# Kernel tuning notes

Measured on AMD Instinct MI355X. Metric: run time of the kernel, lower is better.

The kernel has to match this reference:

```python
import jax, jax.numpy as jnp
import numpy as np

# Module config (init_kwargs)
OUT_H, OUT_W = 7, 7
SPATIAL_SCALE = 0.25
SAMPLE_NUM = 2          # fixed sampling grid (sample_num > 0 branch of mmcv kernel)
ALIGNED = True
CLOCKWISE = False

B, C, H, W = 2, 256, 200, 200
R = 1000


def setup_inputs() -> dict:
    key = jax.random.key(0)
    k1, k2, k3, k4, k5, k6 = jax.random.split(key, 6)
    features = jax.random.normal(k1, (B, C, H, W), dtype=jnp.float32)
    # rois: (batch_index, cx, cy, w, h, angle) in input-image coordinates
    bidx = jax.random.randint(k2, (R,), 0, B).astype(jnp.float32)
    cx = jax.random.uniform(k3, (R,), minval=100.0, maxval=700.0)
    cy = jax.random.uniform(k4, (R,), minval=100.0, maxval=700.0)
    wh = jax.random.uniform(k5, (R, 2), minval=20.0, maxval=200.0)
    ang = jax.random.uniform(k6, (R,), minval=-np.pi, maxval=np.pi)
    rois = jnp.concatenate(
        [bidx[:, None], cx[:, None], cy[:, None], wh, ang[:, None]], axis=1
    ).astype(jnp.float32)
    return {"features": features, "rois": rois}


def _bilinear_gather(features, bidx, y, x):
    """features: [B,C,H,W]; bidx: [R] int; y,x: [R,P] float. Returns [R,P,C]."""
    Hf, Wf = features.shape[2], features.shape[3]
    valid = (y > -1.0) & (y < Hf) & (x > -1.0) & (x < Wf)
    y = jnp.maximum(y, 0.0)
    x = jnp.maximum(x, 0.0)
    yl = jnp.floor(y).astype(jnp.int32)
    xl = jnp.floor(x).astype(jnp.int32)
    ych = yl >= Hf - 1
    xch = xl >= Wf - 1
    yl = jnp.where(ych, Hf - 1, yl)
    yh = jnp.where(ych, Hf - 1, yl + 1)
    xl = jnp.where(xch, Wf - 1, xl)
    xh = jnp.where(xch, Wf - 1, xl + 1)
    ly = jnp.where(ych, 0.0, y - yl.astype(y.dtype))
    lx = jnp.where(xch, 0.0, x - xl.astype(x.dtype))
    hy, hx = 1.0 - ly, 1.0 - lx
    b = bidx[:, None]  # [R,1] broadcast against [R,P]
    v1 = features[b, :, yl, xl]  # [R,P,C]
    v2 = features[b, :, yl, xh]
    v3 = features[b, :, yh, xl]
    v4 = features[b, :, yh, xh]
    val = (hy * hx)[..., None] * v1 + (hy * lx)[..., None] * v2 \
        + (ly * hx)[..., None] * v3 + (ly * lx)[..., None] * v4
    return jnp.where(valid[..., None], val, 0.0)


def _roi_align_rotated(features, rois):
    g = SAMPLE_NUM
    offset = 0.5 if ALIGNED else 0.0
    bidx = rois[:, 0].astype(jnp.int32)
    cx = rois[:, 1] * SPATIAL_SCALE - offset
    cy = rois[:, 2] * SPATIAL_SCALE - offset
    rw = rois[:, 3] * SPATIAL_SCALE
    rh = rois[:, 4] * SPATIAL_SCALE
    theta = -rois[:, 5] if CLOCKWISE else rois[:, 5]
    if not ALIGNED:
        rw = jnp.maximum(rw, 1.0)
        rh = jnp.maximum(rh, 1.0)
    bin_h = rh / OUT_H
    bin_w = rw / OUT_W
    # sample offsets within roi frame, origin at roi center
    ph = jnp.arange(OUT_H, dtype=jnp.float32)
    pw = jnp.arange(OUT_W, dtype=jnp.float32)
    ig = (jnp.arange(g, dtype=jnp.float32) + 0.5) / g
    # yy: [R, OUT_H, g]; xx: [R, OUT_W, g]
    yy = -rh[:, None, None] / 2.0 + (ph[None, :, None] + ig[None, None, :]) * bin_h[:, None, None]
    xx = -rw[:, None, None] / 2.0 + (pw[None, :, None] + ig[None, None, :]) * bin_w[:, None, None]
    # broadcast to [R, OUT_H, OUT_W, g, g]
    yy5 = yy[:, :, None, :, None]
    xx5 = xx[:, None, :, None, :]
    sin_t = jnp.sin(theta)[:, None, None, None, None]
    cos_t = jnp.cos(theta)[:, None, None, None, None]
    x = yy5 * sin_t + xx5 * cos_t + cx[:, None, None, None, None]
    y = yy5 * cos_t - xx5 * sin_t + cy[:, None, None, None, None]
    P = OUT_H * OUT_W * g * g
    vals = _bilinear_gather(features, bidx, y.reshape(R, P), x.reshape(R, P))  # [R,P,C]
    vals = vals.reshape(R, OUT_H, OUT_W, g * g, C).mean(axis=3)  # [R,OUT_H,OUT_W,C]
    return jnp.transpose(vals, (0, 3, 1, 2))  # [R,C,OUT_H,OUT_W]


def reference(features, rois):
    return _roi_align_rotated(features, rois)
```

## Files before the change

### kernel.cpp

```cpp
#include <hip/hip_runtime.h>
#include <math.h>

#define OUT_H 7
#define OUT_W 7
#define GS 2
#define NBINS (OUT_H * OUT_W)
#define NSAMP (GS * GS)
#define NMETA (NBINS * NSAMP)
#define SPATIAL_SCALE 0.25f
#define B_ 2
#define C_ 256
#define H_ 200
#define W_ 200
#define R_ 1000
#define HW_ (H_ * W_)

typedef _Float16 half_t;
typedef __attribute__((ext_vector_type(8))) _Float16 half8;
typedef __attribute__((ext_vector_type(2))) _Float16 half2_t;
typedef __attribute__((ext_vector_type(4))) float f32x4;


__global__ __launch_bounds__(256)
void nchw_to_nhwc_h(const float* __restrict__ in, half_t* __restrict__ out,
                    const float* __restrict__ rois, int* __restrict__ perm) {
    __shared__ float tile[64][64];

    __shared__ int bpos[8][64];
    __shared__ int novf, take;
    __shared__ unsigned char claimed[R_];
    __shared__ short ovf[R_];
    if (blockIdx.x == 0 && blockIdx.y == 0 && blockIdx.z == 0) {
        const int t0 = threadIdx.x;
        for (int i = t0; i < 8 * 64; i += 256) ((int*)bpos)[i] = 0;
        if (t0 == 0) { novf = 0; take = 0; }
        for (int t = t0; t < R_; t += 256) claimed[t] = 0;
        __syncthreads();
        for (int t = t0; t < R_; t += 256) {
            const float* roi = rois + t * 6;
            int   b   = (int)roi[0];
            float cyf = roi[2] * SPATIAL_SCALE;
            float cxf = roi[1] * SPATIAL_SCALE;
            int q = (int)((cyf - 25.0f) * (4.0f / 150.0f));
            q = q < 0 ? 0 : (q > 3 ? 3 : q);
            int band = b * 4 + q;
            band = band < 0 ? 0 : (band > 7 ? 7 : band);
            int bk = (int)((cxf - 25.0f) * (64.0f / 150.0f));
            bk = bk < 0 ? 0 : (bk > 63 ? 63 : bk);
            atomicAdd(&bpos[band][bk], 1);
        }
        __syncthreads();
        if (t0 < 8) {
            int s = 0;
            for (int k = 0; k < 64; ++k) {
                int c = bpos[t0][k];
                bpos[t0][k] = s;
                s += c;
            }
        }
        __syncthreads();
        for (int t = t0; t < R_; t += 256) {
            const float* roi = rois + t * 6;
            int   b   = (int)roi[0];
            float cyf = roi[2] * SPATIAL_SCALE;
            float cxf = roi[1] * SPATIAL_SCALE;
            int q = (int)((cyf - 25.0f) * (4.0f / 150.0f));
            q = q < 0 ? 0 : (q > 3 ? 3 : q);
            int band = b * 4 + q;
            band = band < 0 ? 0 : (band > 7 ? 7 : band);
            int bk = (int)((cxf - 25.0f) * (64.0f / 150.0f));
            bk = bk < 0 ? 0 : (bk > 63 ? 63 : bk);
            int pos = atomicAdd(&bpos[band][bk], 1);
            if (pos < R_ / 8) {
                int id = band + 8 * pos;
                perm[id] = t;
                claimed[id] = 1;
            } else {
                ovf[atomicAdd(&novf, 1)] = (short)t;
            }
        }
        __syncthreads();
        for (int t = t0; t < R_; t += 256) {
            if (!claimed[t]) perm[t] = (int)ovf[atomicAdd(&take, 1)];
        }
    }

    const int hw0 = blockIdx.x * 64;
    const int c0  = blockIdx.y * 64;
    const int b   = blockIdx.z;
    const int t   = threadIdx.x;

    {
        const f32x4* ip4 = (const f32x4*)(in + ((size_t)b * C_ + c0) * HW_ + hw0);
        const int r = t >> 4;
        const int q = t & 15;
#pragma unroll
        for (int k = 0; k < 4; ++k) {
            const int c = r + 16 * k;
            f32x4 v = __builtin_nontemporal_load(&ip4[(size_t)c * (HW_ / 4) + q]);
            const int g = q ^ ((c ^ (c >> 3)) & 7);
            ((f32x4*)tile)[c * 16 + g] = v;
        }
    }
    __syncthreads();
    {
        const int cg = t & 7;
        const int hb = t >> 3;
        half_t* op = out + ((size_t)b * HW_ + hw0) * C_ + c0 + 8 * cg;
#pragma unroll
        for (int i = 0; i < 2; ++i) {
            const int hw = hb + 32 * i;
            const int gh = hw >> 2, oh = hw & 3;
            half8 h;
#pragma unroll
            for (int dc = 0; dc < 8; ++dc) {
                const int c = 8 * cg + dc;
                const float f = tile[c][4 * (gh ^ ((c ^ (c >> 3)) & 7)) + oh];
                h[dc] = (half_t)f;
            }
            *(half8*)(op + (size_t)hw * C_) = h;
        }
    }
}

__device__ __forceinline__ void mix2(float& a0, float& a1,
                                     unsigned int pair, float w) {
    asm("v_fma_mix_f32 %0, %1, %2, %0 op_sel:[0,0,0] op_sel_hi:[1,0,0]"
        : "+v"(a0) : "v"(pair), "v"(w));
    asm("v_fma_mix_f32 %0, %1, %2, %0 op_sel:[1,0,0] op_sel_hi:[1,0,0]"
        : "+v"(a1) : "v"(pair), "v"(w));
}

__device__ __forceinline__ void mix8(float (&a)[8], const uint4& t, float w) {
    mix2(a[0], a[1], t.x, w); mix2(a[2], a[3], t.y, w);
    mix2(a[4], a[5], t.z, w); mix2(a[6], a[7], t.w, w);
}

struct TapsP { uint4 t[8]; };

__device__ __forceinline__ void load_pairs(TapsP& T, const uint4* __restrict__ fp4,
                                           const int2* __restrict__ s_o,
                                           int m, int lane) {
#pragma unroll
    for (int s = 0; s < 4; ++s) {
        const int2 o = s_o[m + s];
        T.t[2 * s + 0] = fp4[o.x + lane];
        T.t[2 * s + 1] = fp4[o.y + lane];
    }
}

__device__ __forceinline__ void fma_store(const TapsP& T,
                                          const float4* __restrict__ s_w,
                                          int m, int j, int lane,
                                          float (&obuf)[8][32][NBINS]) {
    float a[8] = {0.f, 0.f, 0.f, 0.f, 0.f, 0.f, 0.f, 0.f};
    const float2* w2 = ((const float2*)s_w) + (lane >> 5);
#pragma unroll
    for (int s = 0; s < 4; ++s) {
        const float2 ws = w2[2 * (m + s)];
        mix8(a, T.t[2 * s + 0], ws.x);
        mix8(a, T.t[2 * s + 1], ws.y);
    }
#pragma unroll
    for (int k = 0; k < 8; ++k) a[k] += __shfl_xor(a[k], 32, 64);
    if (lane < 32) {
#pragma unroll
        for (int k = 0; k < 8; ++k) obuf[k][lane][j] = a[k];
    }
}

__global__ __launch_bounds__(512, 4)
void gather_nhwc(const half_t* __restrict__ nhwc,
                 const float* __restrict__ rois,
                 const int* __restrict__ perm,
                 float* __restrict__ out) {
    __shared__ float  obuf[8][32][NBINS];
    __shared__ int2   s_o[NMETA];
    __shared__ float4 s_w[NMETA];

    const int r    = perm[blockIdx.x];
    const int tid  = threadIdx.x;
    const int wave = tid >> 6;
    const int lane = tid & 63;

    if (tid < NMETA) {
        const float* roi = rois + r * 6;
        const int   b     = (int)roi[0];
        const float cx    = roi[1] * SPATIAL_SCALE - 0.5f;
        const float cy    = roi[2] * SPATIAL_SCALE - 0.5f;
        const float rw    = roi[3] * SPATIAL_SCALE;
        const float rh    = roi[4] * SPATIAL_SCALE;
        const float theta = roi[5];
        const float bin_h = rh * (1.0f / OUT_H);
        const float bin_w = rw * (1.0f / OUT_W);
        float st, ct;
        __sincosf(theta, &st, &ct);

        const int bin = tid >> 2;
        const int s   = tid & 3;
        const int ph  = bin / OUT_W, pw = bin % OUT_W;
        const int iy  = s >> 1,      ix = s & 1;

        const float yy = -rh * 0.5f + ((float)ph + ((float)iy + 0.5f) * 0.5f) * bin_h;
        const float xx = -rw * 0.5f + ((float)pw + ((float)ix + 0.5f) * 0.5f) * bin_w;
        float x = yy * st + xx * ct + cx;
        float y = yy * ct - xx * st + cy;

        const bool valid = (y > -1.0f) && (y < (float)H_) &&
                           (x > -1.0f) && (x < (float)W_);
        y = fmaxf(y, 0.0f);
        x = fmaxf(x, 0.0f);
        int yl = (int)y, xl = (int)x;
        int yh; float ly;
        if (yl >= H_ - 1) { yl = H_ - 1; yh = H_ - 1; ly = 0.0f; }
        else              { yh = yl + 1; ly = y - (float)yl; }
        int xp; float e0, e1;
        if (xl >= W_ - 1) { xp = W_ - 2; e0 = 0.0f; e1 = 1.0f; }
        else              { xp = xl; const float lx = x - (float)xl;
                            e0 = 1.0f - lx; e1 = lx; }
        const float hy = 1.0f - ly;
        const float scale = valid ? (1.0f / NSAMP) : 0.0f;

        const int bplane = b * HW_;
        s_o[tid] = make_int2((bplane + yl * W_ + xp) * 32,
                             (bplane + yh * W_ + xp) * 32);
        s_w[tid] = make_float4(hy * e0 * scale, ly * e0 * scale,
                               hy * e1 * scale, ly * e1 * scale);
    }
    __syncthreads();

    const uint4* __restrict__ fp4 = (const uint4*)nhwc;

    {
        TapsP A, B;
        int jA = wave;
        int jB = wave + 8;
        load_pairs(A, fp4, s_o, 4 * jA, lane);
        if (jB < NBINS) load_pairs(B, fp4, s_o, 4 * jB, lane);
        __builtin_amdgcn_sched_barrier(0);

        fma_store(A, s_w, 4 * jA, jA, lane, obuf);
        jA += 16;
        if (jA < NBINS) load_pairs(A, fp4, s_o, 4 * jA, lane);
        __builtin_amdgcn_sched_barrier(0);
        if (jB < NBINS) {
            fma_store(B, s_w, 4 * jB, jB, lane, obuf);
            jB += 16;
            if (jB < NBINS) load_pairs(B, fp4, s_o, 4 * jB, lane);
            __builtin_amdgcn_sched_barrier(0);
        }
        if (jA < NBINS) {
            fma_store(A, s_w, 4 * jA, jA, lane, obuf);
            jA += 16;
            if (jA < NBINS) load_pairs(A, fp4, s_o, 4 * jA, lane);
            __builtin_amdgcn_sched_barrier(0);
        }
        if (jB < NBINS) {
            fma_store(B, s_w, 4 * jB, jB, lane, obuf);
            jB += 16;
            if (jB < NBINS) load_pairs(B, fp4, s_o, 4 * jB, lane);
            __builtin_amdgcn_sched_barrier(0);
        }
        if (jA < NBINS) {
            fma_store(A, s_w, 4 * jA, jA, lane, obuf);
            jA += 16;
            if (jA < NBINS) load_pairs(A, fp4, s_o, 4 * jA, lane);
            __builtin_amdgcn_sched_barrier(0);
        }
        if (jB < NBINS) {
            fma_store(B, s_w, 4 * jB, jB, lane, obuf);
            jB += 16;
        }
        if (jA < NBINS) {
            fma_store(A, s_w, 4 * jA, jA, lane, obuf);
        }
    }
    __syncthreads();

    float* out_r = out + (size_t)r * (C_ * NBINS);
    const int E = C_ * NBINS;
#pragma unroll
    for (int i = 0; i < (E + 511) / 512; ++i) {
        const int f = tid + 512 * i;
        if (f < E) {
            const int c = f / NBINS;
            const int j = f - c * NBINS;
            __builtin_nontemporal_store(obuf[c & 7][c >> 3][j], &out_r[f]);
        }
    }
}


struct alignas(16) Samp {
    int o0, o1, o2, o3;
    float w0, w1, w2, w3;
};

__device__ __forceinline__ Samp compute_samp(const float* __restrict__ rois,
                                             int r, int ph, int pw, int s) {
    const float* roi = rois + r * 6;
    int   b     = (int)roi[0];
    float cx    = roi[1] * SPATIAL_SCALE - 0.5f;
    float cy    = roi[2] * SPATIAL_SCALE - 0.5f;
    float rw    = roi[3] * SPATIAL_SCALE;
    float rh    = roi[4] * SPATIAL_SCALE;
    float theta = roi[5];
    float bin_h = rh * (1.0f / OUT_H);
    float bin_w = rw * (1.0f / OUT_W);
    int iy = s / GS, ix = s % GS;
    float yy = -rh * 0.5f + ((float)ph + ((float)iy + 0.5f) * (1.0f / GS)) * bin_h;
    float xx = -rw * 0.5f + ((float)pw + ((float)ix + 0.5f) * (1.0f / GS)) * bin_w;
    float st = sinf(theta), ct = cosf(theta);
    float x = yy * st + xx * ct + cx;
    float y = yy * ct - xx * st + cy;
    bool valid = (y > -1.0f) && (y < (float)H_) && (x > -1.0f) && (x < (float)W_);
    y = fmaxf(y, 0.0f);
    x = fmaxf(x, 0.0f);
    int yl = (int)y;
    int xl = (int)x;
    int yh; float ly;
    if (yl >= H_ - 1) { yl = H_ - 1; yh = H_ - 1; ly = 0.0f; }
    else              { yh = yl + 1; ly = y - (float)yl; }
    int xh; float lx;
    if (xl >= W_ - 1) { xl = W_ - 1; xh = W_ - 1; lx = 0.0f; }
    else              { xh = xl + 1; lx = x - (float)xl; }
    float hy = 1.0f - ly, hx = 1.0f - lx;
    float scale = valid ? (1.0f / NSAMP) : 0.0f;
    Samp sp;
    int base = b * (C_ * H_ * W_);
    sp.o0 = base + yl * W_ + xl;
    sp.o1 = base + yl * W_ + xh;
    sp.o2 = base + yh * W_ + xl;
    sp.o3 = base + yh * W_ + xh;
    sp.w0 = hy * hx * scale;
    sp.w1 = hy * lx * scale;
    sp.w2 = ly * hx * scale;
    sp.w3 = ly * lx * scale;
    return sp;
}

__global__ __launch_bounds__(256)
void mono_kernel(const float* __restrict__ feat,
                 const float* __restrict__ rois,
                 float* __restrict__ out) {
    int tid = blockIdx.x * blockDim.x + threadIdx.x;
    if (tid >= R_ * C_ * NBINS) return;
    int bin = tid % NBINS;
    int rc  = tid / NBINS;
    int c   = rc % C_;
    int r   = rc / C_;
    int coff = c * (H_ * W_);
    float acc = 0.0f;
#pragma unroll
    for (int s = 0; s < NSAMP; ++s) {
        Samp t = compute_samp(rois, r, bin / OUT_W, bin % OUT_W, s);
        acc += t.w0 * feat[coff + t.o0];
        acc += t.w1 * feat[coff + t.o1];
        acc += t.w2 * feat[coff + t.o2];
        acc += t.w3 * feat[coff + t.o3];
    }
    out[tid] = acc;
}


extern "C" void kernel_launch(void* const* d_in, const int* in_sizes, int n_in,
                              void* d_out, int out_size, void* d_ws, size_t ws_size,
                              hipStream_t stream) {
    const float* feat = (const float*)d_in[0];
    const float* rois = (const float*)d_in[1];
    float* out = (float*)d_out;

    const size_t nhwc_bytes = (size_t)B_ * C_ * HW_ * sizeof(half_t);
    const size_t perm_bytes = (size_t)R_ * sizeof(int);

    if (ws_size >= nhwc_bytes + perm_bytes) {
        half_t* nhwc = (half_t*)d_ws;
        int*    perm = (int*)((char*)d_ws + nhwc_bytes);
        dim3 tgrid(HW_ / 64, C_ / 64, B_);
        nchw_to_nhwc_h<<<tgrid, 256, 0, stream>>>(feat, nhwc, rois, perm);
        gather_nhwc<<<R_, 512, 0, stream>>>(nhwc, rois, perm, out);
    } else {
        const int n_out = R_ * C_ * NBINS;
        mono_kernel<<<(n_out + 255) / 256, 256, 0, stream>>>(feat, rois, out);
    }
}
```

Measured before the change: 151.6 us.

## Deduplicate and skip zero-weight bilinear row taps per bin

Per-sample metadata is replaced by per-bin metadata: one thread per output bin computes its four sample points, merges taps that share a row-pair address, and drops taps whose weights are both zero. Only the unique non-zero taps are fetched and accumulated. The goal is fewer global gathers for out-of-bounds or overlapping samples in small ROIs. The cost is a serial dedup loop in 49 threads, variable-length loops with data-dependent branches, and the loss of the explicit software-pipelined double buffering across bins.

```diff
diff --git a/kernel.cpp b/kernel.cpp
--- a/kernel.cpp
+++ b/kernel.cpp
@@ -6,7 +6,6 @@
 #define GS 2
 #define NBINS (OUT_H * OUT_W)
 #define NSAMP (GS * GS)
-#define NMETA (NBINS * NSAMP)
 #define SPATIAL_SCALE 0.25f
 #define B_ 2
 #define C_ 256
@@ -136,54 +135,22 @@
     mix2(a[4], a[5], t.z, w); mix2(a[6], a[7], t.w, w);
 }
 
-struct TapsP { uint4 t[8]; };
-
-__device__ __forceinline__ void load_pairs(TapsP& T, const uint4* __restrict__ fp4,
-                                           const int2* __restrict__ s_o,
-                                           int m, int lane) {
-#pragma unroll
-    for (int s = 0; s < 4; ++s) {
-        const int2 o = s_o[m + s];
-        T.t[2 * s + 0] = fp4[o.x + lane];
-        T.t[2 * s + 1] = fp4[o.y + lane];
-    }
-}
-
-__device__ __forceinline__ void fma_store(const TapsP& T,
-                                          const float4* __restrict__ s_w,
-                                          int m, int j, int lane,
-                                          float (&obuf)[8][32][NBINS]) {
-    float a[8] = {0.f, 0.f, 0.f, 0.f, 0.f, 0.f, 0.f, 0.f};
-    const float2* w2 = ((const float2*)s_w) + (lane >> 5);
-#pragma unroll
-    for (int s = 0; s < 4; ++s) {
-        const float2 ws = w2[2 * (m + s)];
-        mix8(a, T.t[2 * s + 0], ws.x);
-        mix8(a, T.t[2 * s + 1], ws.y);
-    }
-#pragma unroll
-    for (int k = 0; k < 8; ++k) a[k] += __shfl_xor(a[k], 32, 64);
-    if (lane < 32) {
-#pragma unroll
-        for (int k = 0; k < 8; ++k) obuf[k][lane][j] = a[k];
-    }
-}
-
 __global__ __launch_bounds__(512, 4)
 void gather_nhwc(const half_t* __restrict__ nhwc,
                  const float* __restrict__ rois,
                  const int* __restrict__ perm,
                  float* __restrict__ out) {
     __shared__ float  obuf[8][32][NBINS];
-    __shared__ int2   s_o[NMETA];
-    __shared__ float4 s_w[NMETA];
+    __shared__ int    s_cnt[NBINS];
+    __shared__ int    s_off[NBINS][8];
+    __shared__ float2 s_w[NBINS][8];
 
     const int r    = perm[blockIdx.x];
     const int tid  = threadIdx.x;
     const int wave = tid >> 6;
     const int lane = tid & 63;
 
-    if (tid < NMETA) {
+    if (tid < NBINS) {
         const float* roi = rois + r * 6;
         const int   b     = (int)roi[0];
         const float cx    = roi[1] * SPATIAL_SCALE - 0.5f;
@@ -196,83 +163,101 @@
         float st, ct;
         __sincosf(theta, &st, &ct);
 
-        const int bin = tid >> 2;
-        const int s   = tid & 3;
-        const int ph  = bin / OUT_W, pw = bin % OUT_W;
-        const int iy  = s >> 1,      ix = s & 1;
-
-        const float yy = -rh * 0.5f + ((float)ph + ((float)iy + 0.5f) * 0.5f) * bin_h;
-        const float xx = -rw * 0.5f + ((float)pw + ((float)ix + 0.5f) * 0.5f) * bin_w;
-        float x = yy * st + xx * ct + cx;
-        float y = yy * ct - xx * st + cy;
-
-        const bool valid = (y > -1.0f) && (y < (float)H_) &&
-                           (x > -1.0f) && (x < (float)W_);
-        y = fmaxf(y, 0.0f);
-        x = fmaxf(x, 0.0f);
-        int yl = (int)y, xl = (int)x;
-        int yh; float ly;
-        if (yl >= H_ - 1) { yl = H_ - 1; yh = H_ - 1; ly = 0.0f; }
-        else              { yh = yl + 1; ly = y - (float)yl; }
-        int xp; float e0, e1;
-        if (xl >= W_ - 1) { xp = W_ - 2; e0 = 0.0f; e1 = 1.0f; }
-        else              { xp = xl; const float lx = x - (float)xl;
-                            e0 = 1.0f - lx; e1 = lx; }
-        const float hy = 1.0f - ly;
-        const float scale = valid ? (1.0f / NSAMP) : 0.0f;
-
+        const int ph = tid / OUT_W, pw = tid % OUT_W;
         const int bplane = b * HW_;
-        s_o[tid] = make_int2((bplane + yl * W_ + xp) * 32,
-                             (bplane + yh * W_ + xp) * 32);
-        s_w[tid] = make_float4(hy * e0 * scale, ly * e0 * scale,
-                               hy * e1 * scale, ly * e1 * scale);
+
+        int   offs[8];
+        float w0a[8], w1a[8];
+        int n = 0;
+#pragma unroll
+        for (int s = 0; s < NSAMP; ++s) {
+            const int iy = s >> 1, ix = s & 1;
+            const float yy = -rh * 0.5f + ((float)ph + ((float)iy + 0.5f) * 0.5f) * bin_h;
+            const float xx = -rw * 0.5f + ((float)pw + ((float)ix + 0.5f) * 0.5f) * bin_w;
+            float x = yy * st + xx * ct + cx;
+            float y = yy * ct - xx * st + cy;
+
+            const bool valid = (y > -1.0f) && (y < (float)H_) &&
+                               (x > -1.0f) && (x < (float)W_);
+            y = fmaxf(y, 0.0f);
+            x = fmaxf(x, 0.0f);
+            int yl = (int)y, xl = (int)x;
+            int yh; float ly;
+            if (yl >= H_ - 1) { yl = H_ - 1; yh = H_ - 1; ly = 0.0f; }
+            else              { yh = yl + 1; ly = y - (float)yl; }
+            int xp; float e0, e1;
+            if (xl >= W_ - 1) { xp = W_ - 2; e0 = 0.0f; e1 = 1.0f; }
+            else              { xp = xl; const float lx = x - (float)xl;
+                                e0 = 1.0f - lx; e1 = lx; }
+            const float hy = 1.0f - ly;
+            const float scale = valid ? (1.0f / NSAMP) : 0.0f;
+
+            const int   ro[2] = { (bplane + yl * W_ + xp) * 32,
+                                  (bplane + yh * W_ + xp) * 32 };
+            const float wy[2] = { hy, ly };
+            for (int h = 0; h < 2; ++h) {
+                const float w0 = wy[h] * e0 * scale;
+                const float w1 = wy[h] * e1 * scale;
+                if (w0 == 0.0f && w1 == 0.0f) continue;
+                int f = -1;
+                for (int k = 0; k < n; ++k)
+                    if (offs[k] == ro[h]) { f = k; break; }
+                if (f >= 0) { w0a[f] += w0; w1a[f] += w1; }
+                else        { offs[n] = ro[h]; w0a[n] = w0; w1a[n] = w1; ++n; }
+            }
+        }
+        s_cnt[tid] = n;
+        for (int k = 0; k < n; ++k) {
+            s_off[tid][k] = offs[k];
+            s_w[tid][k]   = make_float2(w0a[k], w1a[k]);
+        }
     }
     __syncthreads();
 
     const uint4* __restrict__ fp4 = (const uint4*)nhwc;
 
-    {
-        TapsP A, B;
-        int jA = wave;
-        int jB = wave + 8;
-        load_pairs(A, fp4, s_o, 4 * jA, lane);
-        if (jB < NBINS) load_pairs(B, fp4, s_o, 4 * jB, lane);
+    for (int j = wave; j < NBINS; j += 16) {
+        const int j2 = j + 8;
+        const int nA = s_cnt[j];
+        const int nB = (j2 < NBINS) ? s_cnt[j2] : 0;
+        uint4 tA[8], tB[8];
+#pragma unroll
+        for (int k = 0; k < 8; ++k)
+            if (k < nA) tA[k] = fp4[s_off[j][k] + lane];
+#pragma unroll
+        for (int k = 0; k < 8; ++k)
+            if (k < nB) tB[k] = fp4[s_off[j2][k] + lane];
         __builtin_amdgcn_sched_barrier(0);
 
-        fma_store(A, s_w, 4 * jA, jA, lane, obuf);
-        jA += 16;
-        if (jA < NBINS) load_pairs(A, fp4, s_o, 4 * jA, lane);
-        __builtin_amdgcn_sched_barrier(0);
-        if (jB < NBINS) {
-            fma_store(B, s_w, 4 * jB, jB, lane, obuf);
-            jB += 16;
-            if (jB < NBINS) load_pairs(B, fp4, s_o, 4 * jB, lane);
-            __builtin_amdgcn_sched_barrier(0);
-        }
-        if (jA < NBINS) {
-            fma_store(A, s_w, 4 * jA, jA, lane, obuf);
-            jA += 16;
-            if (jA < NBINS) load_pairs(A, fp4, s_o, 4 * jA, lane);
-            __builtin_amdgcn_sched_barrier(0);
-        }
-        if (jB < NBINS) {
-            fma_store(B, s_w, 4 * jB, jB, lane, obuf);
-            jB += 16;
-            if (jB < NBINS) load_pairs(B, fp4, s_o, 4 * jB, lane);
-            __builtin_amdgcn_sched_barrier(0);
-        }
-        if (jA < NBINS) {
-            fma_store(A, s_w, 4 * jA, jA, lane, obuf);
-            jA += 16;
-            if (jA < NBINS) load_pairs(A, fp4, s_o, 4 * jA, lane);
-            __builtin_amdgcn_sched_barrier(0);
-        }
-        if (jB < NBINS) {
-            fma_store(B, s_w, 4 * jB, jB, lane, obuf);
-            jB += 16;
-        }
-        if (jA < NBINS) {
-            fma_store(A, s_w, 4 * jA, jA, lane, obuf);
+        {
+            float a[8] = {0.f, 0.f, 0.f, 0.f, 0.f, 0.f, 0.f, 0.f};
+#pragma unroll
+            for (int k = 0; k < 8; ++k)
+                if (k < nA) {
+                    const float2 w = s_w[j][k];
+                    mix8(a, tA[k], (lane & 32) ? w.y : w.x);
+                }
+#pragma unroll
+            for (int k = 0; k < 8; ++k) a[k] += __shfl_xor(a[k], 32, 64);
+            if (lane < 32) {
+#pragma unroll
+                for (int k = 0; k < 8; ++k) obuf[k][lane][j] = a[k];
+            }
+        }
+        if (j2 < NBINS) {
+            float a[8] = {0.f, 0.f, 0.f, 0.f, 0.f, 0.f, 0.f, 0.f};
+#pragma unroll
+            for (int k = 0; k < 8; ++k)
+                if (k < nB) {
+                    const float2 w = s_w[j2][k];
+                    mix8(a, tB[k], (lane & 32) ? w.y : w.x);
+                }
+#pragma unroll
+            for (int k = 0; k < 8; ++k) a[k] += __shfl_xor(a[k], 32, 64);
+            if (lane < 32) {
+#pragma unroll
+                for (int k = 0; k < 8; ++k) obuf[k][lane][j2] = a[k];
+            }
         }
     }
     __syncthreads();
```

Result: slower. 195.1 us (+28.7%).
